# Performance work log

Hardware: AMD Instinct MI355X
Metric: run time of the kernel (lower is better)

## Reference

```python
import jax, jax.numpy as jnp
import numpy as np

B, S, E, H = 1, 4096, 768, 12
D = E // H  # head_dim = 64


def setup_inputs() -> dict:
    key = jax.random.key(0)
    ks = jax.random.split(key, 6)
    scale = 0.02
    x = jax.random.normal(ks[0], (B, S, E), dtype=jnp.float32)
    Wq = jax.random.normal(ks[1], (E, E), dtype=jnp.float32) * scale
    Wk = jax.random.normal(ks[2], (E, E), dtype=jnp.float32) * scale
    Wv = jax.random.normal(ks[3], (E, E), dtype=jnp.float32) * scale
    Wo = jax.random.normal(ks[4], (E, E), dtype=jnp.float32) * scale
    bo = jax.random.normal(ks[5], (E,), dtype=jnp.float32) * scale
    mask = jnp.tril(jnp.ones((S, S), dtype=bool))[None, None]  # [1,1,S,S] causal
    return {"x": x, "Wq": Wq, "Wk": Wk, "Wv": Wv, "Wo": Wo, "bo": bo, "mask": mask}


def reference(x, Wq, Wk, Wv, Wo, bo, mask):
    # projections (torch Linear: y = x @ W.T; here W stored as [E,E] applied as x@W)
    q = jnp.einsum('bse,ef->bsf', x, Wq).reshape(B, S, H, D).transpose(0, 2, 1, 3)
    k = jnp.einsum('bse,ef->bsf', x, Wk).reshape(B, S, H, D).transpose(0, 2, 1, 3)
    v = jnp.einsum('bse,ef->bsf', x, Wv).reshape(B, S, H, D).transpose(0, 2, 1, 3)
    scores = jnp.einsum('bhqd,bhkd->bhqk', q, k) / jnp.sqrt(jnp.float32(D))
    scores = jnp.where(mask, scores, -jnp.inf)
    attn = jax.nn.softmax(scores, axis=-1)  # dropout p=0 -> identity
    ctx = jnp.einsum('bhqk,bhkd->bhqd', attn, v)
    ctx = ctx.transpose(0, 2, 1, 3).reshape(B, S, E)
    return jnp.einsum('bse,ef->bsf', ctx, Wo) + bo
```

## Files before the change

kernel.cpp:

```cpp
#include <hip/hip_runtime.h>
#include <math.h>

#define S 4096
#define E 768
#define H 12
#define Dh 64
#define SCALE2 0.1803368801111204f

typedef short short8 __attribute__((ext_vector_type(8)));
typedef float floatx4 __attribute__((ext_vector_type(4)));

__device__ __forceinline__ unsigned short f2bf(float f) {
    union { float f; unsigned int i; } c; c.f = f;
    unsigned int i = c.i;
    return (unsigned short)((i + 0x7fffu + ((i >> 16) & 1u)) >> 16);
}

__device__ __forceinline__ unsigned int pk_bf16(float lo, float hi) {
#if __has_builtin(__builtin_amdgcn_cvt_pk_bf16_f32)
    typedef __bf16 bf16x2 __attribute__((ext_vector_type(2)));
    union { bf16x2 v; unsigned int u; } c;
    c.v = __builtin_amdgcn_cvt_pk_bf16_f32(lo, hi);
    return c.u;
#else
    union { float f; unsigned int i; } a, b; a.f = lo; b.f = hi;
    return ((a.i + 0x8000u) >> 16) | ((b.i + 0x8000u) & 0xFFFF0000u);
#endif
}

__device__ __forceinline__ void gload_lds16(const unsigned short* g, unsigned short* l) {
    __builtin_amdgcn_global_load_lds(
        (const __attribute__((address_space(1))) unsigned int*)g,
        (__attribute__((address_space(3))) unsigned int*)l, 16, 0, 0);
}

__global__ __launch_bounds__(256)
void prep_kernel(const float* __restrict__ x, unsigned short* __restrict__ xb,
                 const float* __restrict__ s0, const float* __restrict__ s1,
                 const float* __restrict__ s2, const float* __restrict__ s3,
                 unsigned short* __restrict__ d0, unsigned short* __restrict__ d1,
                 unsigned short* __restrict__ d2, unsigned short* __restrict__ d3) {
    __shared__ unsigned short tile[32][33];
    const int b = blockIdx.x;
    const int tid = threadIdx.x;
    if (b < 2304) {
        int z = b / 576, rem = b - z * 576;
        int bx = rem % 24, by = rem / 24;
        const float* src = (z == 0) ? s0 : (z == 1) ? s1 : (z == 2) ? s2 : s3;
        unsigned short* dst = (z == 0) ? d0 : (z == 1) ? d1 : (z == 2) ? d2 : d3;
        int tx = tid & 31, ty = tid >> 5;
        int xcol = bx * 32 + tx;
        int y0 = by * 32;
        for (int j = ty; j < 32; j += 8)
            tile[j][tx] = f2bf(src[(size_t)(y0 + j) * E + xcol]);
        __syncthreads();
        int x2 = y0 + tx;
        int y2 = bx * 32;
        for (int j = ty; j < 32; j += 8)
            dst[(size_t)(y2 + j) * E + x2] = tile[tx][j];
    } else {
        int i = ((b - 2304) * 256 + tid) * 8;
        float4 f0 = *reinterpret_cast<const float4*>(x + i);
        float4 f1 = *reinterpret_cast<const float4*>(x + i + 4);
        unsigned short u[8];
        u[0]=f2bf(f0.x); u[1]=f2bf(f0.y); u[2]=f2bf(f0.z); u[3]=f2bf(f0.w);
        u[4]=f2bf(f1.x); u[5]=f2bf(f1.y); u[6]=f2bf(f1.z); u[7]=f2bf(f1.w);
        *reinterpret_cast<uint4*>(xb + i) = *reinterpret_cast<uint4*>(u);
    }
}

__global__ __launch_bounds__(256)
void gemm_qkv(const unsigned short* __restrict__ A,
              const unsigned short* __restrict__ BT,
              unsigned short* __restrict__ Qb, unsigned short* __restrict__ Kb,
              unsigned short* __restrict__ VTb) {
    __shared__ unsigned short Asm[128 * 64];
    __shared__ unsigned short Bsm[64 * 64];
    const int tid  = threadIdx.x;
    const int wave = tid >> 6, lane = tid & 63;
    const int quad = lane >> 4, l16 = lane & 15;
    const int lrow = lane >> 3, lchunk = lane & 7;
    const int bb = blockIdx.x;
    const int xcd = bb & 7, j = bb >> 3;
    const int mt = (xcd >> 1) * 8 + (j & 7);
    const int nt = (xcd & 1) * 18 + (j >> 3);
    const int n0 = nt * 64;
    const int m0 = mt * 128;

    floatx4 acc[2][4];
    #pragma unroll
    for (int at = 0; at < 2; at++)
        #pragma unroll
        for (int ct = 0; ct < 4; ct++)
            #pragma unroll
            for (int r = 0; r < 4; r++) acc[at][ct][r] = 0.f;

    for (int k0 = 0; k0 < E; k0 += 64) {
        #pragma unroll
        for (int i = 0; i < 4; i++) {
            int rbase = wave * 32 + i * 8;
            int row   = rbase + lrow;
            int gc    = lchunk ^ (row & 7);
            gload_lds16(&A[(size_t)(m0 + row) * E + k0 + gc * 8], &Asm[rbase * 64]);
        }
        #pragma unroll
        for (int i = 0; i < 2; i++) {
            int rbase = wave * 16 + i * 8;
            int row   = rbase + lrow;
            int gc    = lchunk ^ (row & 7);
            gload_lds16(&BT[(size_t)(n0 + row) * E + k0 + gc * 8], &Bsm[rbase * 64]);
        }
        __syncthreads();
        #pragma unroll
        for (int kk = 0; kk < 2; kk++) {
            const int g = kk * 4 + quad;
            short8 af[2], bfr[4];
            #pragma unroll
            for (int t = 0; t < 2; t++) {
                int ar = wave * 32 + t * 16 + l16;
                af[t] = *reinterpret_cast<const short8*>(&Asm[ar * 64 + (g ^ (ar & 7)) * 8]);
            }
            #pragma unroll
            for (int ct = 0; ct < 4; ct++) {
                int br = ct * 16 + l16;
                bfr[ct] = *reinterpret_cast<const short8*>(&Bsm[br * 64 + (g ^ (br & 7)) * 8]);
            }
            #pragma unroll
            for (int at = 0; at < 2; at++)
                #pragma unroll
                for (int ct = 0; ct < 4; ct++)
                    acc[at][ct] = __builtin_amdgcn_mfma_f32_16x16x32_bf16(af[at], bfr[ct], acc[at][ct], 0, 0, 0);
        }
        __syncthreads();
    }

    const int sec = n0 / 768;
    const int nb  = n0 - sec * 768;
    #pragma unroll
    for (int at = 0; at < 2; at++)
        #pragma unroll
        for (int ct = 0; ct < 4; ct++) {
            int nsec = nb + ct * 16 + l16, hh = nsec >> 6, d = nsec & 63;
            #pragma unroll
            for (int r = 0; r < 4; r++) {
                int s = m0 + wave * 32 + at * 16 + quad * 4 + r;
                float v = acc[at][ct][r];
                if (sec == 0)      Qb [(size_t)hh * S * Dh + (size_t)s * Dh + d] = f2bf(v * SCALE2);
                else if (sec == 1) Kb [(size_t)hh * S * Dh + (size_t)s * Dh + d] = f2bf(v);
                else               VTb[(size_t)hh * Dh * S + (size_t)d * S + s]  = f2bf(v);
            }
        }
}

__global__ __launch_bounds__(256)
void gemm_out(const float* __restrict__ ctxf,
              const unsigned short* __restrict__ BT,
              const float* __restrict__ lsumf,
              float* __restrict__ outp, const float* __restrict__ bias) {
    __shared__ unsigned short Asm[128 * 64];
    __shared__ unsigned short Bsm[64 * 64];
    const int tid  = threadIdx.x;
    const int wave = tid >> 6, lane = tid & 63;
    const int quad = lane >> 4, l16 = lane & 15;
    const int lrow = lane >> 3, lchunk = lane & 7;
    const int bb = blockIdx.x;
    const int xcd = bb & 7, j = bb >> 3;
    const int mt = (xcd >> 1) * 8 + (j & 7);
    const int nt = (xcd & 1) * 6 + (j >> 3);
    const int n0 = nt * 64;
    const int m0 = mt * 128;
    const int arow = tid >> 1, ahalf = tid & 1;

    floatx4 acc[2][4];
    #pragma unroll
    for (int at = 0; at < 2; at++)
        #pragma unroll
        for (int ct = 0; ct < 4; ct++)
            #pragma unroll
            for (int r = 0; r < 4; r++) acc[at][ct][r] = 0.f;

    for (int k0 = 0; k0 < E; k0 += 64) {
        {
            const float* asrc = ctxf + (size_t)(m0 + arow) * E + k0 + ahalf * 32;
            float linv = 1.0f / lsumf[(k0 >> 6) * S + m0 + arow];
            #pragma unroll
            for (int hf = 0; hf < 2; hf++) {
                float4 fa = *reinterpret_cast<const float4*>(asrc + hf * 16);
                float4 fb = *reinterpret_cast<const float4*>(asrc + hf * 16 + 4);
                float4 fc = *reinterpret_cast<const float4*>(asrc + hf * 16 + 8);
                float4 fd = *reinterpret_cast<const float4*>(asrc + hf * 16 + 12);
                uint4 w0, w1;
                w0.x = pk_bf16(fa.x * linv, fa.y * linv); w0.y = pk_bf16(fa.z * linv, fa.w * linv);
                w0.z = pk_bf16(fb.x * linv, fb.y * linv); w0.w = pk_bf16(fb.z * linv, fb.w * linv);
                w1.x = pk_bf16(fc.x * linv, fc.y * linv); w1.y = pk_bf16(fc.z * linv, fc.w * linv);
                w1.z = pk_bf16(fd.x * linv, fd.y * linv); w1.w = pk_bf16(fd.z * linv, fd.w * linv);
                int c0 = ahalf * 4 + hf * 2;
                *reinterpret_cast<uint4*>(&Asm[arow * 64 + ((c0    ) ^ (arow & 7)) * 8]) = w0;
                *reinterpret_cast<uint4*>(&Asm[arow * 64 + ((c0 + 1) ^ (arow & 7)) * 8]) = w1;
            }
        }
        #pragma unroll
        for (int i = 0; i < 2; i++) {
            int rbase = wave * 16 + i * 8;
            int row   = rbase + lrow;
            int gc    = lchunk ^ (row & 7);
            gload_lds16(&BT[(size_t)(n0 + row) * E + k0 + gc * 8], &Bsm[rbase * 64]);
        }
        __syncthreads();
        #pragma unroll
        for (int kk = 0; kk < 2; kk++) {
            const int g = kk * 4 + quad;
            short8 af[2], bfr[4];
            #pragma unroll
            for (int t = 0; t < 2; t++) {
                int ar = wave * 32 + t * 16 + l16;
                af[t] = *reinterpret_cast<const short8*>(&Asm[ar * 64 + (g ^ (ar & 7)) * 8]);
            }
            #pragma unroll
            for (int ct = 0; ct < 4; ct++) {
                int br = ct * 16 + l16;
                bfr[ct] = *reinterpret_cast<const short8*>(&Bsm[br * 64 + (g ^ (br & 7)) * 8]);
            }
            #pragma unroll
            for (int at = 0; at < 2; at++)
                #pragma unroll
                for (int ct = 0; ct < 4; ct++)
                    acc[at][ct] = __builtin_amdgcn_mfma_f32_16x16x32_bf16(af[at], bfr[ct], acc[at][ct], 0, 0, 0);
        }
        __syncthreads();
    }

    #pragma unroll
    for (int at = 0; at < 2; at++)
        #pragma unroll
        for (int ct = 0; ct < 4; ct++) {
            int n = n0 + ct * 16 + l16;
            float bn = bias[n];
            #pragma unroll
            for (int r = 0; r < 4; r++) {
                int s = m0 + wave * 32 + at * 16 + quad * 4 + r;
                outp[(size_t)s * E + n] = acc[at][ct][r] + bn;
            }
        }
}

__global__ __launch_bounds__(256)
void attn_kernel(const unsigned short* __restrict__ Q,
                 const unsigned short* __restrict__ K,
                 const unsigned short* __restrict__ VT,
                 float* __restrict__ ctxf,
                 float* __restrict__ lsumf) {
    __shared__ unsigned short Ksm[64 * 64];
    __shared__ unsigned short Vsm[64 * 64];
    __shared__ unsigned short P[4][2][16][72];
    const int tid  = threadIdx.x;
    const int wave = tid >> 6, lane = tid & 63;
    const int quad = lane >> 4, l16 = lane & 15;
    const int lrow = lane >> 3, lchunk = lane & 7;

    const int b = blockIdx.x;
    const int w = b / H;
    const int h = b - w * H;
    int Qb, ck, nck;
    if (w < 32)       { Qb = 31 - (w >> 3);       ck = w & 7;         nck = 8; }
    else if (w < 60)  { int u = w - 32;  Qb = 27 - u / 7;  ck = u % 7; nck = 7; }
    else if (w < 84)  { int u = w - 60;  Qb = 23 - u / 6;  ck = u % 6; nck = 6; }
    else if (w < 104) { int u = w - 84;  Qb = 19 - u / 5;  ck = u % 5; nck = 5; }
    else if (w < 120) { int u = w - 104; Qb = 15 - (u >> 2); ck = u & 3; nck = 4; }
    else if (w < 132) { int u = w - 120; Qb = 11 - u / 3;  ck = u % 3; nck = 3; }
    else if (w < 140) { int u = w - 132; Qb = 7 - (u >> 1); ck = u & 1; nck = 2; }
    else              { Qb = 3 - (w - 140);       ck = 0;             nck = 1; }
    const int ntiles = 2 * Qb + 2;
    const int kt0 = (ntiles * ck) / nck;
    const int kt1 = (ntiles * (ck + 1)) / nck;

    const int qs = Qb * 128 + wave * 32;

    const unsigned short* Qh = Q  + (size_t)h * S * Dh;
    const unsigned short* Kh = K  + (size_t)h * S * Dh;
    const unsigned short* Vh = VT + (size_t)h * Dh * S;

    short8 bq[2][2];
    #pragma unroll
    for (int st = 0; st < 2; st++)
        #pragma unroll
        for (int c = 0; c < 2; c++)
            bq[st][c] = *reinterpret_cast<const short8*>(
                &Qh[(size_t)(qs + st * 16 + l16) * Dh + c * 32 + quad * 8]);

    float lsum[2] = {0.f, 0.f};
    floatx4 o[2][4];
    #pragma unroll
    for (int st = 0; st < 2; st++)
        #pragma unroll
        for (int ct = 0; ct < 4; ct++)
            #pragma unroll
            for (int r = 0; r < 4; r++) o[st][ct][r] = 0.f;

    for (int kt = kt0; kt < kt1; kt++) {
        #pragma unroll
        for (int i = 0; i < 2; i++) {
            int rbase = wave * 16 + i * 8;
            int row   = rbase + lrow;
            int gc    = lchunk ^ (row & 7);
            gload_lds16(&Kh[(size_t)(kt * 64 + row) * Dh + gc * 8], &Ksm[rbase * 64]);
            gload_lds16(&Vh[(size_t)row * S + kt * 64 + gc * 8],    &Vsm[rbase * 64]);
        }
        __syncthreads();

        floatx4 sc[2][4];
        #pragma unroll
        for (int st = 0; st < 2; st++)
            #pragma unroll
            for (int ct = 0; ct < 4; ct++)
                #pragma unroll
                for (int r = 0; r < 4; r++) sc[st][ct][r] = 0.f;
        #pragma unroll
        for (int c = 0; c < 2; c++)
            #pragma unroll
            for (int ct = 0; ct < 4; ct++) {
                int kr = ct * 16 + l16;
                short8 ak = *reinterpret_cast<const short8*>(
                    &Ksm[kr * 64 + ((c * 4 + quad) ^ (kr & 7)) * 8]);
                sc[0][ct] = __builtin_amdgcn_mfma_f32_16x16x32_bf16(ak, bq[0][c], sc[0][ct], 0, 0, 0);
                sc[1][ct] = __builtin_amdgcn_mfma_f32_16x16x32_bf16(ak, bq[1][c], sc[1][ct], 0, 0, 0);
            }

        if (kt >= 2 * Qb) {
            #pragma unroll
            for (int st = 0; st < 2; st++) {
                int qrow = qs + st * 16 + l16;
                #pragma unroll
                for (int ct = 0; ct < 4; ct++)
                    #pragma unroll
                    for (int r = 0; r < 4; r++) {
                        int kcol = kt * 64 + ct * 16 + quad * 4 + r;
                        if (kcol > qrow) sc[st][ct][r] = -INFINITY;
                    }
            }
        }

        #pragma unroll
        for (int st = 0; st < 2; st++)
            #pragma unroll
            for (int ct = 0; ct < 4; ct++) {
                float pv[4];
                #pragma unroll
                for (int r = 0; r < 4; r++) {
                    float p = __builtin_amdgcn_exp2f(sc[st][ct][r]);
                    lsum[st] += p;
                    pv[r] = p;
                }
                uint2 w2;
                w2.x = pk_bf16(pv[0], pv[1]);
                w2.y = pk_bf16(pv[2], pv[3]);
                *reinterpret_cast<uint2*>(&P[wave][st][l16][ct * 16 + quad * 4]) = w2;
            }
        __asm__ volatile("s_waitcnt lgkmcnt(0)" ::: "memory");

        #pragma unroll
        for (int c = 0; c < 2; c++) {
            short8 ap0 = *reinterpret_cast<const short8*>(&P[wave][0][l16][c * 32 + quad * 8]);
            short8 ap1 = *reinterpret_cast<const short8*>(&P[wave][1][l16][c * 32 + quad * 8]);
            #pragma unroll
            for (int ct = 0; ct < 4; ct++) {
                int vr = ct * 16 + l16;
                short8 bv = *reinterpret_cast<const short8*>(
                    &Vsm[vr * 64 + ((c * 4 + quad) ^ (vr & 7)) * 8]);
                o[0][ct] = __builtin_amdgcn_mfma_f32_16x16x32_bf16(ap0, bv, o[0][ct], 0, 0, 0);
                o[1][ct] = __builtin_amdgcn_mfma_f32_16x16x32_bf16(ap1, bv, o[1][ct], 0, 0, 0);
            }
        }
        __syncthreads();
    }

    #pragma unroll
    for (int st = 0; st < 2; st++) {
        lsum[st] += __shfl_xor(lsum[st], 16, 64);
        lsum[st] += __shfl_xor(lsum[st], 32, 64);
    }
    if (quad == 0) {
        #pragma unroll
        for (int st = 0; st < 2; st++)
            atomicAdd(&lsumf[h * S + qs + st * 16 + l16], lsum[st]);
    }
    #pragma unroll
    for (int st = 0; st < 2; st++)
        #pragma unroll
        for (int r = 0; r < 4; r++) {
            int s = qs + st * 16 + quad * 4 + r;
            #pragma unroll
            for (int ct = 0; ct < 4; ct++)
                atomicAdd(&ctxf[(size_t)s * E + h * Dh + ct * 16 + l16], o[st][ct][r]);
        }
}

extern "C" void kernel_launch(void* const* d_in, const int* in_sizes, int n_in,
                              void* d_out, int out_size, void* d_ws, size_t ws_size,
                              hipStream_t stream) {
    const float* x  = (const float*)d_in[0];
    const float* Wq = (const float*)d_in[1];
    const float* Wk = (const float*)d_in[2];
    const float* Wv = (const float*)d_in[3];
    const float* Wo = (const float*)d_in[4];
    const float* bo = (const float*)d_in[5];
    float* out = (float*)d_out;

    char* ws = (char*)d_ws;
    const size_t WT = (size_t)E * E * 2;
    const size_t QB = (size_t)S * E * 2;
    unsigned short* WqT = (unsigned short*)(ws + 0 * WT);
    unsigned short* WkT = (unsigned short*)(ws + 1 * WT);
    unsigned short* WvT = (unsigned short*)(ws + 2 * WT);
    unsigned short* WoT = (unsigned short*)(ws + 3 * WT);
    unsigned short* xb  = (unsigned short*)(ws + 4 * WT + 0 * QB);
    unsigned short* Qbf = (unsigned short*)(ws + 4 * WT + 1 * QB);
    unsigned short* Kbf = (unsigned short*)(ws + 4 * WT + 2 * QB);
    unsigned short* VTb = (unsigned short*)(ws + 4 * WT + 3 * QB);
    float*          ctxf  = (float*)(ws + 4 * WT + 4 * QB);
    float*          lsumf = (float*)(ws + 4 * WT + 4 * QB + (size_t)S * E * 4);

    hipMemsetAsync(ctxf, 0, (size_t)S * E * 4 + (size_t)H * S * 4, stream);

    prep_kernel<<<2304 + (S * E) / (256 * 8), 256, 0, stream>>>(
        x, xb, Wq, Wk, Wv, Wo, WqT, WkT, WvT, WoT);

    gemm_qkv<<<1152, 256, 0, stream>>>(xb, WqT, Qbf, Kbf, VTb);

    attn_kernel<<<1728, 256, 0, stream>>>(Qbf, Kbf, VTb, ctxf, lsumf);

    gemm_out<<<384, 256, 0, stream>>>(ctxf, WoT, lsumf, out, bo);
}
```

Measured before the change: 252.3 us.

## Fold zeroing into prep, enlarge QKV tiles, double-buffer attention, split ctx normalization

Several changes land at once. The memset is folded into extra blocks of the prep kernel, and the QKV GEMM tile grows to 128x128 with a 2x2 wave layout, halving the grid. The attention kernel double-buffers its K/V LDS tiles so the next tile loads while the current one computes. Context normalization and bf16 conversion move into a separate kernel, so gemm_out can load A directly into LDS. The tradeoffs are an extra launch and extra ctx round-trip traffic, more LDS per attention block, and higher register pressure in the QKV GEMM.

```diff
diff --git a/kernel.cpp b/kernel.cpp
--- a/kernel.cpp
+++ b/kernel.cpp
@@ -39,7 +39,8 @@
                  const float* __restrict__ s0, const float* __restrict__ s1,
                  const float* __restrict__ s2, const float* __restrict__ s3,
                  unsigned short* __restrict__ d0, unsigned short* __restrict__ d1,
-                 unsigned short* __restrict__ d2, unsigned short* __restrict__ d3) {
+                 unsigned short* __restrict__ d2, unsigned short* __restrict__ d3,
+                 float* __restrict__ zbase) {
     __shared__ unsigned short tile[32][33];
     const int b = blockIdx.x;
     const int tid = threadIdx.x;
@@ -58,7 +59,7 @@
         int y2 = bx * 32;
         for (int j = ty; j < 32; j += 8)
             dst[(size_t)(y2 + j) * E + x2] = tile[tx][j];
-    } else {
+    } else if (b < 3840) {
         int i = ((b - 2304) * 256 + tid) * 8;
         float4 f0 = *reinterpret_cast<const float4*>(x + i);
         float4 f1 = *reinterpret_cast<const float4*>(x + i + 4);
@@ -66,6 +67,13 @@
         u[0]=f2bf(f0.x); u[1]=f2bf(f0.y); u[2]=f2bf(f0.z); u[3]=f2bf(f0.w);
         u[4]=f2bf(f1.x); u[5]=f2bf(f1.y); u[6]=f2bf(f1.z); u[7]=f2bf(f1.w);
         *reinterpret_cast<uint4*>(xb + i) = *reinterpret_cast<uint4*>(u);
+    } else {
+        size_t i = ((size_t)(b - 3840) * 256 + tid) * 16;
+        float4 z4 = make_float4(0.f, 0.f, 0.f, 0.f);
+        *reinterpret_cast<float4*>(zbase + i)      = z4;
+        *reinterpret_cast<float4*>(zbase + i + 4)  = z4;
+        *reinterpret_cast<float4*>(zbase + i + 8)  = z4;
+        *reinterpret_cast<float4*>(zbase + i + 12) = z4;
     }
 }
 
@@ -75,7 +83,7 @@
               unsigned short* __restrict__ Qb, unsigned short* __restrict__ Kb,
               unsigned short* __restrict__ VTb) {
     __shared__ unsigned short Asm[128 * 64];
-    __shared__ unsigned short Bsm[64 * 64];
+    __shared__ unsigned short Bsm[128 * 64];
     const int tid  = threadIdx.x;
     const int wave = tid >> 6, lane = tid & 63;
     const int quad = lane >> 4, l16 = lane & 15;
@@ -83,13 +91,14 @@
     const int bb = blockIdx.x;
     const int xcd = bb & 7, j = bb >> 3;
     const int mt = (xcd >> 1) * 8 + (j & 7);
-    const int nt = (xcd & 1) * 18 + (j >> 3);
-    const int n0 = nt * 64;
+    const int nt = (xcd & 1) * 9 + (j >> 3);
+    const int n0 = nt * 128;
     const int m0 = mt * 128;
-
-    floatx4 acc[2][4];
-    #pragma unroll
-    for (int at = 0; at < 2; at++)
+    const int aw = wave >> 1, bw = wave & 1;
+
+    floatx4 acc[4][4];
+    #pragma unroll
+    for (int at = 0; at < 4; at++)
         #pragma unroll
         for (int ct = 0; ct < 4; ct++)
             #pragma unroll
@@ -101,32 +110,23 @@
             int rbase = wave * 32 + i * 8;
             int row   = rbase + lrow;
             int gc    = lchunk ^ (row & 7);
-            gload_lds16(&A[(size_t)(m0 + row) * E + k0 + gc * 8], &Asm[rbase * 64]);
-        }
-        #pragma unroll
-        for (int i = 0; i < 2; i++) {
-            int rbase = wave * 16 + i * 8;
-            int row   = rbase + lrow;
-            int gc    = lchunk ^ (row & 7);
+            gload_lds16(&A [(size_t)(m0 + row) * E + k0 + gc * 8], &Asm[rbase * 64]);
             gload_lds16(&BT[(size_t)(n0 + row) * E + k0 + gc * 8], &Bsm[rbase * 64]);
         }
         __syncthreads();
         #pragma unroll
         for (int kk = 0; kk < 2; kk++) {
             const int g = kk * 4 + quad;
-            short8 af[2], bfr[4];
-            #pragma unroll
-            for (int t = 0; t < 2; t++) {
-                int ar = wave * 32 + t * 16 + l16;
-                af[t] = *reinterpret_cast<const short8*>(&Asm[ar * 64 + (g ^ (ar & 7)) * 8]);
-            }
-            #pragma unroll
-            for (int ct = 0; ct < 4; ct++) {
-                int br = ct * 16 + l16;
-                bfr[ct] = *reinterpret_cast<const short8*>(&Bsm[br * 64 + (g ^ (br & 7)) * 8]);
-            }
-            #pragma unroll
-            for (int at = 0; at < 2; at++)
+            short8 af[4], bfr[4];
+            #pragma unroll
+            for (int t = 0; t < 4; t++) {
+                int ar = aw * 64 + t * 16 + l16;
+                af[t]  = *reinterpret_cast<const short8*>(&Asm[ar * 64 + (g ^ (ar & 7)) * 8]);
+                int br = bw * 64 + t * 16 + l16;
+                bfr[t] = *reinterpret_cast<const short8*>(&Bsm[br * 64 + (g ^ (br & 7)) * 8]);
+            }
+            #pragma unroll
+            for (int at = 0; at < 4; at++)
                 #pragma unroll
                 for (int ct = 0; ct < 4; ct++)
                     acc[at][ct] = __builtin_amdgcn_mfma_f32_16x16x32_bf16(af[at], bfr[ct], acc[at][ct], 0, 0, 0);
@@ -135,15 +135,15 @@
     }
 
     const int sec = n0 / 768;
-    const int nb  = n0 - sec * 768;
-    #pragma unroll
-    for (int at = 0; at < 2; at++)
+    const int nb  = n0 - sec * 768 + bw * 64;
+    #pragma unroll
+    for (int at = 0; at < 4; at++)
         #pragma unroll
         for (int ct = 0; ct < 4; ct++) {
             int nsec = nb + ct * 16 + l16, hh = nsec >> 6, d = nsec & 63;
             #pragma unroll
             for (int r = 0; r < 4; r++) {
-                int s = m0 + wave * 32 + at * 16 + quad * 4 + r;
+                int s = m0 + aw * 64 + at * 16 + quad * 4 + r;
                 float v = acc[at][ct][r];
                 if (sec == 0)      Qb [(size_t)hh * S * Dh + (size_t)s * Dh + d] = f2bf(v * SCALE2);
                 else if (sec == 1) Kb [(size_t)hh * S * Dh + (size_t)s * Dh + d] = f2bf(v);
@@ -153,9 +153,24 @@
 }
 
 __global__ __launch_bounds__(256)
-void gemm_out(const float* __restrict__ ctxf,
+void normctx(const float* __restrict__ ctxf, const float* __restrict__ lsumf,
+             unsigned short* __restrict__ ctxb) {
+    int i = (blockIdx.x * 256 + threadIdx.x) * 8;
+    int s = i / E, e = i - s * E;
+    float linv = 1.0f / lsumf[(e >> 6) * S + s];
+    float4 f0 = *reinterpret_cast<const float4*>(ctxf + i);
+    float4 f1 = *reinterpret_cast<const float4*>(ctxf + i + 4);
+    uint4 w;
+    w.x = pk_bf16(f0.x * linv, f0.y * linv);
+    w.y = pk_bf16(f0.z * linv, f0.w * linv);
+    w.z = pk_bf16(f1.x * linv, f1.y * linv);
+    w.w = pk_bf16(f1.z * linv, f1.w * linv);
+    *reinterpret_cast<uint4*>(ctxb + i) = w;
+}
+
+__global__ __launch_bounds__(256)
+void gemm_out(const unsigned short* __restrict__ A,
               const unsigned short* __restrict__ BT,
-              const float* __restrict__ lsumf,
               float* __restrict__ outp, const float* __restrict__ bias) {
     __shared__ unsigned short Asm[128 * 64];
     __shared__ unsigned short Bsm[64 * 64];
@@ -169,7 +184,6 @@
     const int nt = (xcd & 1) * 6 + (j >> 3);
     const int n0 = nt * 64;
     const int m0 = mt * 128;
-    const int arow = tid >> 1, ahalf = tid & 1;
 
     floatx4 acc[2][4];
     #pragma unroll
@@ -180,24 +194,12 @@
             for (int r = 0; r < 4; r++) acc[at][ct][r] = 0.f;
 
     for (int k0 = 0; k0 < E; k0 += 64) {
-        {
-            const float* asrc = ctxf + (size_t)(m0 + arow) * E + k0 + ahalf * 32;
-            float linv = 1.0f / lsumf[(k0 >> 6) * S + m0 + arow];
-            #pragma unroll
-            for (int hf = 0; hf < 2; hf++) {
-                float4 fa = *reinterpret_cast<const float4*>(asrc + hf * 16);
-                float4 fb = *reinterpret_cast<const float4*>(asrc + hf * 16 + 4);
-                float4 fc = *reinterpret_cast<const float4*>(asrc + hf * 16 + 8);
-                float4 fd = *reinterpret_cast<const float4*>(asrc + hf * 16 + 12);
-                uint4 w0, w1;
-                w0.x = pk_bf16(fa.x * linv, fa.y * linv); w0.y = pk_bf16(fa.z * linv, fa.w * linv);
-                w0.z = pk_bf16(fb.x * linv, fb.y * linv); w0.w = pk_bf16(fb.z * linv, fb.w * linv);
-                w1.x = pk_bf16(fc.x * linv, fc.y * linv); w1.y = pk_bf16(fc.z * linv, fc.w * linv);
-                w1.z = pk_bf16(fd.x * linv, fd.y * linv); w1.w = pk_bf16(fd.z * linv, fd.w * linv);
-                int c0 = ahalf * 4 + hf * 2;
-                *reinterpret_cast<uint4*>(&Asm[arow * 64 + ((c0    ) ^ (arow & 7)) * 8]) = w0;
-                *reinterpret_cast<uint4*>(&Asm[arow * 64 + ((c0 + 1) ^ (arow & 7)) * 8]) = w1;
-            }
+        #pragma unroll
+        for (int i = 0; i < 4; i++) {
+            int rbase = wave * 32 + i * 8;
+            int row   = rbase + lrow;
+            int gc    = lchunk ^ (row & 7);
+            gload_lds16(&A[(size_t)(m0 + row) * E + k0 + gc * 8], &Asm[rbase * 64]);
         }
         #pragma unroll
         for (int i = 0; i < 2; i++) {
@@ -250,8 +252,8 @@
                  const unsigned short* __restrict__ VT,
                  float* __restrict__ ctxf,
                  float* __restrict__ lsumf) {
-    __shared__ unsigned short Ksm[64 * 64];
-    __shared__ unsigned short Vsm[64 * 64];
+    __shared__ unsigned short Ksm[2][64 * 64];
+    __shared__ unsigned short Vsm[2][64 * 64];
     __shared__ unsigned short P[4][2][16][72];
     const int tid  = threadIdx.x;
     const int wave = tid >> 6, lane = tid & 63;
@@ -297,16 +299,23 @@
             #pragma unroll
             for (int r = 0; r < 4; r++) o[st][ct][r] = 0.f;
 
-    for (int kt = kt0; kt < kt1; kt++) {
+    auto stage = [&](int kt, int buf) {
         #pragma unroll
         for (int i = 0; i < 2; i++) {
             int rbase = wave * 16 + i * 8;
             int row   = rbase + lrow;
             int gc    = lchunk ^ (row & 7);
-            gload_lds16(&Kh[(size_t)(kt * 64 + row) * Dh + gc * 8], &Ksm[rbase * 64]);
-            gload_lds16(&Vh[(size_t)row * S + kt * 64 + gc * 8],    &Vsm[rbase * 64]);
-        }
-        __syncthreads();
+            gload_lds16(&Kh[(size_t)(kt * 64 + row) * Dh + gc * 8], &Ksm[buf][rbase * 64]);
+            gload_lds16(&Vh[(size_t)row * S + kt * 64 + gc * 8],    &Vsm[buf][rbase * 64]);
+        }
+    };
+
+    stage(kt0, 0);
+    __syncthreads();
+
+    for (int kt = kt0; kt < kt1; kt++) {
+        const int cur = (kt - kt0) & 1;
+        if (kt + 1 < kt1) stage(kt + 1, cur ^ 1);
 
         floatx4 sc[2][4];
         #pragma unroll
@@ -321,7 +330,7 @@
             for (int ct = 0; ct < 4; ct++) {
                 int kr = ct * 16 + l16;
                 short8 ak = *reinterpret_cast<const short8*>(
-                    &Ksm[kr * 64 + ((c * 4 + quad) ^ (kr & 7)) * 8]);
+                    &Ksm[cur][kr * 64 + ((c * 4 + quad) ^ (kr & 7)) * 8]);
                 sc[0][ct] = __builtin_amdgcn_mfma_f32_16x16x32_bf16(ak, bq[0][c], sc[0][ct], 0, 0, 0);
                 sc[1][ct] = __builtin_amdgcn_mfma_f32_16x16x32_bf16(ak, bq[1][c], sc[1][ct], 0, 0, 0);
             }
@@ -366,7 +375,7 @@
             for (int ct = 0; ct < 4; ct++) {
                 int vr = ct * 16 + l16;
                 short8 bv = *reinterpret_cast<const short8*>(
-                    &Vsm[vr * 64 + ((c * 4 + quad) ^ (vr & 7)) * 8]);
+                    &Vsm[cur][vr * 64 + ((c * 4 + quad) ^ (vr & 7)) * 8]);
                 o[0][ct] = __builtin_amdgcn_mfma_f32_16x16x32_bf16(ap0, bv, o[0][ct], 0, 0, 0);
                 o[1][ct] = __builtin_amdgcn_mfma_f32_16x16x32_bf16(ap1, bv, o[1][ct], 0, 0, 0);
             }
@@ -419,15 +428,17 @@
     unsigned short* VTb = (unsigned short*)(ws + 4 * WT + 3 * QB);
     float*          ctxf  = (float*)(ws + 4 * WT + 4 * QB);
     float*          lsumf = (float*)(ws + 4 * WT + 4 * QB + (size_t)S * E * 4);
-
-    hipMemsetAsync(ctxf, 0, (size_t)S * E * 4 + (size_t)H * S * 4, stream);
-
-    prep_kernel<<<2304 + (S * E) / (256 * 8), 256, 0, stream>>>(
-        x, xb, Wq, Wk, Wv, Wo, WqT, WkT, WvT, WoT);
-
-    gemm_qkv<<<1152, 256, 0, stream>>>(xb, WqT, Qbf, Kbf, VTb);
+    unsigned short* ctxb  = (unsigned short*)(ws + 4 * WT + 4 * QB
+                                              + (size_t)S * E * 4 + (size_t)H * S * 4);
+
+    prep_kernel<<<4656, 256, 0, stream>>>(
+        x, xb, Wq, Wk, Wv, Wo, WqT, WkT, WvT, WoT, ctxf);
+
+    gemm_qkv<<<576, 256, 0, stream>>>(xb, WqT, Qbf, Kbf, VTb);
 
     attn_kernel<<<1728, 256, 0, stream>>>(Qbf, Kbf, VTb, ctxf, lsumf);
 
-    gemm_out<<<384, 256, 0, stream>>>(ctxf, WoT, lsumf, out, bo);
-}
+    normctx<<<(S * E) / (256 * 8), 256, 0, stream>>>(ctxf, lsumf, ctxb);
+
+    gemm_out<<<384, 256, 0, stream>>>(ctxb, WoT, out, bo);
+}
```

After: 250.8 us. Within noise of the previous version (-0.6%).
